# Performance work log

Measured on AMD Instinct MI355X. Metric: run time of the kernel, lower is better.

The kernel has to match this reference:

```python
import jax, jax.numpy as jnp
import numpy as np

N_NODES = 50000
N_EDGES = 800000
NODE_DIM = 128
EDGE_DIM = 64
HID = 2 * NODE_DIM + EDGE_DIM  # 320


def setup_inputs() -> dict:
    key = jax.random.key(0)
    k1, k2, k3, k4 = jax.random.split(key, 4)
    x = jax.random.normal(k1, (N_NODES, NODE_DIM), dtype=jnp.float32)
    edge_index = jax.random.randint(k2, (2, N_EDGES), 0, N_NODES, dtype=jnp.int32)
    edge_ft = jax.random.normal(k3, (N_EDGES, EDGE_DIM), dtype=jnp.float32)
    kw1, kw2 = jax.random.split(k4)
    scale = 1.0 / np.sqrt(HID)
    W_val = jax.random.uniform(kw1, (NODE_DIM, HID), jnp.float32, -scale, scale)
    b_val = jnp.zeros((NODE_DIM,), jnp.float32)
    W_mul = jax.random.uniform(kw2, (NODE_DIM, HID), jnp.float32, -scale, scale)
    b_mul = jnp.zeros((NODE_DIM,), jnp.float32)
    return {"x": x, "edge_index": edge_index, "edge_ft": edge_ft,
            "W_val": W_val, "b_val": b_val, "W_mul": W_mul, "b_mul": b_mul}


def reference(x, edge_index, edge_ft, W_val, b_val, W_mul, b_mul):
    sender, receiver = edge_index[0], edge_index[1]
    # gather + concat: [E, 2*node_dim + edge_dim]
    c = jnp.concatenate([x[sender], x[receiver], edge_ft], axis=1)
    vals = jax.nn.softplus(c @ W_val.T + b_val)
    gate = jax.nn.sigmoid(c @ W_mul.T + b_mul)
    msg = vals * gate  # [E, node_dim]
    # scatter-sum by receiver into [N, node_dim]
    return jax.ops.segment_sum(msg, receiver, num_segments=x.shape[0])
```

## Files before the change

### kernel.cpp

```cpp
#include <hip/hip_runtime.h>
#include <hip/hip_bf16.h>

#define E_EDGES   800000
#define NN_NODES  50000
#define NODE_DIM  128
#define EDGE_DIM  64
#define KDIM      320
#define NTOT      256
#define BM        128
#define BK        64
#define SA        72
#define THREADS   512

typedef _Float16 half8 __attribute__((ext_vector_type(8)));
typedef float    f32x4 __attribute__((ext_vector_type(4)));

__device__ __forceinline__ unsigned short f2h(float f) {
    _Float16 h = (_Float16)f;
    return __builtin_bit_cast(unsigned short, h);
}

__global__ void cast_all_kernel(const float* __restrict__ x,
                                const float* __restrict__ wv,
                                const float* __restrict__ wm,
                                unsigned short* __restrict__ xh,
                                unsigned short* __restrict__ wc) {
    const int n4x = (NN_NODES * NODE_DIM) / 4;
    const int n4h = (NODE_DIM * KDIM) / 4;
    int i = blockIdx.x * blockDim.x + threadIdx.x;
    const float* src;
    unsigned short* dst;
    int j;
    if (i < n4x) { src = x; dst = xh; j = i; }
    else {
        int k = i - n4x;
        if (k >= 2 * n4h) return;
        dst = wc; j = k;
        src = (k < n4h) ? wv : wm;
        if (k >= n4h) { src = wm; j = k - n4h; }
        dst = wc;
        float4 f = ((const float4*)src)[j];
        ushort4 o;
        o.x = f2h(f.x); o.y = f2h(f.y); o.z = f2h(f.z); o.w = f2h(f.w);
        ((ushort4*)wc)[k] = o;
        return;
    }
    float4 f = ((const float4*)src)[j];
    ushort4 o;
    o.x = f2h(f.x); o.y = f2h(f.y); o.z = f2h(f.z); o.w = f2h(f.w);
    ((ushort4*)dst)[j] = o;
}

__global__ void __launch_bounds__(THREADS, 4)
cgc_main(const unsigned short* __restrict__ xh,
         const int* __restrict__ ei,
         const float* __restrict__ ef,
         const unsigned short* __restrict__ Wc,
         const float* __restrict__ bval,
         const float* __restrict__ bmul,
         float* __restrict__ out)
{
    __shared__ unsigned short As[BM * SA];
    __shared__ unsigned short Bs[NTOT * SA];
    __shared__ int sIdx[BM];
    __shared__ int rIdx[BM];

    const int tid  = threadIdx.x;
    const int e0   = blockIdx.x * BM;
    const int lane = tid & 63;
    const int wid  = tid >> 6;
    const int wm   = wid & 1;
    const int wn   = wid >> 1;
    const int q    = lane >> 4;
    const int l16  = lane & 15;

    if (tid < BM) {
        sIdx[tid] = ei[e0 + tid];
        rIdx[tid] = ei[E_EDGES + e0 + tid];
    }

    f32x4 acc[4][4];
    const f32x4 zero4 = {0.f, 0.f, 0.f, 0.f};
#pragma unroll
    for (int mt = 0; mt < 4; ++mt)
#pragma unroll
        for (int nt = 0; nt < 4; ++nt) acc[mt][nt] = zero4;

    for (int c = 0; c < 5; ++c) {
        __syncthreads();
        if (c < 4) {
            const int kcol = (c & 1) * 64;
#pragma unroll
            for (int i = 0; i < 2; ++i) {
                int u = tid + i * THREADS;
                int row = u >> 3, seg = u & 7;
                int node = (c < 2) ? sIdx[row] : rIdx[row];
                uint4 v = *(const uint4*)(xh + (size_t)node * NODE_DIM + kcol + seg * 8);
                *(uint4*)(&As[row * SA + seg * 8]) = v;
            }
        } else {
#pragma unroll
            for (int i = 0; i < 2; ++i) {
                int u = tid + i * THREADS;
                int row = u >> 3, seg = u & 7;
                const float* s = ef + (size_t)(e0 + row) * EDGE_DIM + seg * 8;
                float4 f0 = ((const float4*)s)[0];
                float4 f1 = ((const float4*)s)[1];
                uint4 v;
                v.x = (unsigned)f2h(f0.x) | ((unsigned)f2h(f0.y) << 16);
                v.y = (unsigned)f2h(f0.z) | ((unsigned)f2h(f0.w) << 16);
                v.z = (unsigned)f2h(f1.x) | ((unsigned)f2h(f1.y) << 16);
                v.w = (unsigned)f2h(f1.z) | ((unsigned)f2h(f1.w) << 16);
                *(uint4*)(&As[row * SA + seg * 8]) = v;
            }
        }
        {
            const int kOff = c * BK;
#pragma unroll
            for (int i = 0; i < 4; ++i) {
                int u = tid + i * THREADS;
                int n = u >> 3, seg = u & 7;
                uint4 v = *(const uint4*)(Wc + n * KDIM + kOff + seg * 8);
                *(uint4*)(&Bs[n * SA + seg * 8]) = v;
            }
        }
        __syncthreads();
#pragma unroll
        for (int ks = 0; ks < BK; ks += 32) {
            half8 a[4], b[4];
#pragma unroll
            for (int mt = 0; mt < 4; ++mt)
                a[mt] = *(const half8*)(&As[(wm * 64 + mt * 16 + l16) * SA + ks + q * 8]);
            const int nb0 = wn * 32;
            const int nbase[4] = { nb0, nb0 + 16, 128 + nb0, 128 + nb0 + 16 };
#pragma unroll
            for (int nt = 0; nt < 4; ++nt)
                b[nt] = *(const half8*)(&Bs[(nbase[nt] + l16) * SA + ks + q * 8]);
#pragma unroll
            for (int mt = 0; mt < 4; ++mt)
#pragma unroll
                for (int nt = 0; nt < 4; ++nt)
                    acc[mt][nt] = __builtin_amdgcn_mfma_f32_16x16x32_f16(
                        a[mt], b[nt], acc[mt][nt], 0, 0, 0);
        }
    }

#pragma unroll
    for (int ct = 0; ct < 2; ++ct) {
        const int col = wn * 32 + ct * 16 + l16;
        const float bv = bval[col];
        const float bm = bmul[col];
#pragma unroll
        for (int mt = 0; mt < 4; ++mt) {
#pragma unroll
            for (int r = 0; r < 4; ++r) {
                float v = acc[mt][ct][r] + bv;
                float g = acc[mt][ct + 2][r] + bm;
                float sp  = fmaxf(v, 0.f) + __logf(1.f + __expf(-fabsf(v)));
                float sig = __builtin_amdgcn_rcpf(1.f + __expf(-g));
                float msg = sp * sig;
                int rl = wm * 64 + mt * 16 + q * 4 + r;
                int node = rIdx[rl];
                atomicAdd(out + (size_t)node * NODE_DIM + col, msg);
            }
        }
    }
}

extern "C" void kernel_launch(void* const* d_in, const int* in_sizes, int n_in,
                              void* d_out, int out_size, void* d_ws, size_t ws_size,
                              hipStream_t stream) {
    const float* x  = (const float*)d_in[0];
    const int*   ei = (const int*)d_in[1];
    const float* ef = (const float*)d_in[2];
    const float* Wv = (const float*)d_in[3];
    const float* bv = (const float*)d_in[4];
    const float* Wm = (const float*)d_in[5];
    const float* bm = (const float*)d_in[6];
    float* out = (float*)d_out;

    unsigned short* xh = (unsigned short*)d_ws;
    unsigned short* Wc = (unsigned short*)((char*)d_ws + 12800000);

    hipMemsetAsync(d_out, 0, (size_t)NN_NODES * NODE_DIM * sizeof(float), stream);

    const int n4x = (NN_NODES * NODE_DIM) / 4;
    const int n4w = (2 * NODE_DIM * KDIM) / 4;
    const int total = n4x + n4w;
    cast_all_kernel<<<(total + 255) / 256, 256, 0, stream>>>(x, Wv, Wm, xh, Wc);

    cgc_main<<<E_EDGES / BM, THREADS, 0, stream>>>(xh, ei, ef, Wc, bv, bm, out);
}
```

Measured before the change: 598.6 us.

## Precompute per-node projections and gather them instead of per-edge node GEMM

Splits the linear layer so that the sender and receiver parts of both projections are computed once per node (50k nodes) in a new pcompute kernel and stored as interleaved fp16 values. The edge kernel then runs only the 64-wide edge-feature GEMM and gathers two precomputed 512-byte rows per edge, adding them before softplus and sigmoid. This removes most of the per-edge MFMA work and the per-block weight staging. In exchange it needs a 51 MB workspace, adds an extra fp16 rounding of the per-node partial sums, and keeps the old path as a fallback when the workspace is too small.

```diff
diff --git a/kernel.cpp b/kernel.cpp
--- a/kernel.cpp
+++ b/kernel.cpp
@@ -1,5 +1,4 @@
 #include <hip/hip_runtime.h>
-#include <hip/hip_bf16.h>
 
 #define E_EDGES   800000
 #define NN_NODES  50000
@@ -7,9 +6,11 @@
 #define EDGE_DIM  64
 #define KDIM      320
 #define NTOT      256
-#define BM        128
-#define BK        64
+#define BM        64
+#define OBM       128
+#define BN        64
 #define SA        72
+#define SX        136
 #define THREADS   512
 
 typedef _Float16 half8 __attribute__((ext_vector_type(8)));
@@ -19,6 +20,205 @@
     _Float16 h = (_Float16)f;
     return __builtin_bit_cast(unsigned short, h);
 }
+__device__ __forceinline__ float h2f(unsigned short u) {
+    return (float)__builtin_bit_cast(_Float16, u);
+}
+
+
+__global__ void cast_w(const float* __restrict__ wv,
+                       const float* __restrict__ wm,
+                       unsigned short* __restrict__ Wc) {
+    const int n4h = (NODE_DIM * KDIM) / 4;
+    int i = blockIdx.x * blockDim.x + threadIdx.x;
+    if (i >= 2 * n4h) return;
+    const float* src = (i < n4h) ? wv : wm;
+    int j = (i < n4h) ? i : i - n4h;
+    float4 f = ((const float4*)src)[j];
+    ushort4 o;
+    o.x = f2h(f.x); o.y = f2h(f.y); o.z = f2h(f.z); o.w = f2h(f.w);
+    ((ushort4*)Wc)[i] = o;
+}
+
+__global__ void __launch_bounds__(THREADS, 4)
+pcompute(const float* __restrict__ x,
+         const unsigned short* __restrict__ Wc,
+         const float* __restrict__ bval,
+         const float* __restrict__ bmul,
+         unsigned short* __restrict__ Ph)
+{
+    __shared__ unsigned short Xs[BN * SX];
+    const int tid  = threadIdx.x;
+    const int n0   = blockIdx.x * BN;
+    const int lane = tid & 63;
+    const int wid  = tid >> 6;
+    const int wm   = wid & 1;
+    const int wn   = wid >> 1;
+    const int q    = lane >> 4;
+    const int l16  = lane & 15;
+
+#pragma unroll
+    for (int i = 0; i < 2; ++i) {
+        int u = tid + i * THREADS;
+        int row = u >> 4, seg = u & 15;
+        int node = n0 + row;
+        if (node >= NN_NODES) node = NN_NODES - 1;
+        const float* s = x + (size_t)node * NODE_DIM + seg * 8;
+        float4 f0 = ((const float4*)s)[0];
+        float4 f1 = ((const float4*)s)[1];
+        uint4 v;
+        v.x = (unsigned)f2h(f0.x) | ((unsigned)f2h(f0.y) << 16);
+        v.y = (unsigned)f2h(f0.z) | ((unsigned)f2h(f0.w) << 16);
+        v.z = (unsigned)f2h(f1.x) | ((unsigned)f2h(f1.y) << 16);
+        v.w = (unsigned)f2h(f1.z) | ((unsigned)f2h(f1.w) << 16);
+        *(uint4*)(&Xs[row * SX + seg * 8]) = v;
+    }
+    __syncthreads();
+
+#pragma unroll
+    for (int nhalf = 0; nhalf < 2; ++nhalf) {
+        f32x4 acc[2][4];
+        const f32x4 zero4 = {0.f, 0.f, 0.f, 0.f};
+#pragma unroll
+        for (int mt = 0; mt < 2; ++mt)
+#pragma unroll
+            for (int nt = 0; nt < 4; ++nt) acc[mt][nt] = zero4;
+
+#pragma unroll
+        for (int ks = 0; ks < 4; ++ks) {
+            half8 a[2], b[4];
+#pragma unroll
+            for (int mt = 0; mt < 2; ++mt)
+                a[mt] = *(const half8*)(&Xs[(wm * 32 + mt * 16 + l16) * SX + ks * 32 + q * 8]);
+#pragma unroll
+            for (int nt = 0; nt < 4; ++nt)
+                b[nt] = *(const half8*)(Wc + (size_t)(wn * 64 + nt * 16 + l16) * KDIM
+                                           + nhalf * 128 + ks * 32 + q * 8);
+#pragma unroll
+            for (int mt = 0; mt < 2; ++mt)
+#pragma unroll
+                for (int nt = 0; nt < 4; ++nt)
+                    acc[mt][nt] = __builtin_amdgcn_mfma_f32_16x16x32_f16(
+                        a[mt], b[nt], acc[mt][nt], 0, 0, 0);
+        }
+
+#pragma unroll
+        for (int mt = 0; mt < 2; ++mt) {
+#pragma unroll
+            for (int nt = 0; nt < 4; ++nt) {
+                int j  = wn * 64 + nt * 16 + l16;
+                int c  = j & 127;
+                int vg = j >> 7;
+                float bb = 0.f;
+                if (nhalf == 0) bb = vg ? bmul[c] : bval[c];
+#pragma unroll
+                for (int r = 0; r < 4; ++r) {
+                    int node = n0 + wm * 32 + mt * 16 + q * 4 + r;
+                    if (node < NN_NODES)
+                        Ph[(size_t)node * 512 + nhalf * 256 + c * 2 + vg] =
+                            f2h(acc[mt][nt][r] + bb);
+                }
+            }
+        }
+    }
+}
+
+__global__ void __launch_bounds__(THREADS, 4)
+cgc_main(const unsigned short* __restrict__ Ph,
+         const int* __restrict__ ei,
+         const float* __restrict__ ef,
+         const unsigned short* __restrict__ Wc,
+         float* __restrict__ out)
+{
+    __shared__ unsigned short As[BM * SA];
+    __shared__ int sIdx[BM];
+    __shared__ int rIdx[BM];
+
+    const int tid  = threadIdx.x;
+    const int e0   = blockIdx.x * BM;
+    const int lane = tid & 63;
+    const int wid  = tid >> 6;
+    const int wm   = wid & 1;
+    const int wn   = wid >> 1;
+    const int q    = lane >> 4;
+    const int l16  = lane & 15;
+
+    if (tid < BM) {
+        sIdx[tid] = ei[e0 + tid];
+        rIdx[tid] = ei[E_EDGES + e0 + tid];
+    }
+
+    {
+        int row = tid >> 3, seg = tid & 7;
+        const float* s = ef + (size_t)(e0 + row) * EDGE_DIM + seg * 8;
+        float4 f0 = ((const float4*)s)[0];
+        float4 f1 = ((const float4*)s)[1];
+        uint4 v;
+        v.x = (unsigned)f2h(f0.x) | ((unsigned)f2h(f0.y) << 16);
+        v.y = (unsigned)f2h(f0.z) | ((unsigned)f2h(f0.w) << 16);
+        v.z = (unsigned)f2h(f1.x) | ((unsigned)f2h(f1.y) << 16);
+        v.w = (unsigned)f2h(f1.z) | ((unsigned)f2h(f1.w) << 16);
+        *(uint4*)(&As[row * SA + seg * 8]) = v;
+    }
+
+    const int nb0 = wn * 32;
+    const int nbase[4] = { nb0, nb0 + 16, 128 + nb0, 128 + nb0 + 16 };
+    half8 b[2][4];
+#pragma unroll
+    for (int ks = 0; ks < 2; ++ks)
+#pragma unroll
+        for (int nt = 0; nt < 4; ++nt)
+            b[ks][nt] = *(const half8*)(Wc + (size_t)(nbase[nt] + l16) * KDIM
+                                           + 256 + ks * 32 + q * 8);
+
+    f32x4 acc[2][4];
+    const f32x4 zero4 = {0.f, 0.f, 0.f, 0.f};
+#pragma unroll
+    for (int mt = 0; mt < 2; ++mt)
+#pragma unroll
+        for (int nt = 0; nt < 4; ++nt) acc[mt][nt] = zero4;
+
+    __syncthreads();
+
+#pragma unroll
+    for (int ks = 0; ks < 2; ++ks) {
+        half8 a[2];
+#pragma unroll
+        for (int mt = 0; mt < 2; ++mt)
+            a[mt] = *(const half8*)(&As[(wm * 32 + mt * 16 + l16) * SA + ks * 32 + q * 8]);
+#pragma unroll
+        for (int mt = 0; mt < 2; ++mt)
+#pragma unroll
+            for (int nt = 0; nt < 4; ++nt)
+                acc[mt][nt] = __builtin_amdgcn_mfma_f32_16x16x32_f16(
+                    a[mt], b[ks][nt], acc[mt][nt], 0, 0, 0);
+    }
+
+#pragma unroll
+    for (int mt = 0; mt < 2; ++mt) {
+#pragma unroll
+        for (int r = 0; r < 4; ++r) {
+            int row = wm * 32 + mt * 16 + q * 4 + r;
+            int sN = sIdx[row];
+            int rN = rIdx[row];
+            const unsigned* pS = (const unsigned*)(Ph + (size_t)sN * 512);
+            const unsigned* pR = (const unsigned*)(Ph + (size_t)rN * 512 + 256);
+#pragma unroll
+            for (int ct = 0; ct < 2; ++ct) {
+                int c = wn * 32 + ct * 16 + l16;
+                unsigned us = pS[c];
+                unsigned ur = pR[c];
+                float v = acc[mt][ct][r]     + h2f((unsigned short)(us & 0xffff))
+                                             + h2f((unsigned short)(ur & 0xffff));
+                float g = acc[mt][ct + 2][r] + h2f((unsigned short)(us >> 16))
+                                             + h2f((unsigned short)(ur >> 16));
+                float sp  = fmaxf(v, 0.f) + __logf(1.f + __expf(-fabsf(v)));
+                float sig = __builtin_amdgcn_rcpf(1.f + __expf(-g));
+                atomicAdd(out + (size_t)rN * NODE_DIM + c, sp * sig);
+            }
+        }
+    }
+}
+
 
 __global__ void cast_all_kernel(const float* __restrict__ x,
                                 const float* __restrict__ wv,
@@ -28,45 +228,39 @@
     const int n4x = (NN_NODES * NODE_DIM) / 4;
     const int n4h = (NODE_DIM * KDIM) / 4;
     int i = blockIdx.x * blockDim.x + threadIdx.x;
-    const float* src;
-    unsigned short* dst;
-    int j;
-    if (i < n4x) { src = x; dst = xh; j = i; }
-    else {
+    if (i < n4x) {
+        float4 f = ((const float4*)x)[i];
+        ushort4 o;
+        o.x = f2h(f.x); o.y = f2h(f.y); o.z = f2h(f.z); o.w = f2h(f.w);
+        ((ushort4*)xh)[i] = o;
+    } else {
         int k = i - n4x;
         if (k >= 2 * n4h) return;
-        dst = wc; j = k;
-        src = (k < n4h) ? wv : wm;
-        if (k >= n4h) { src = wm; j = k - n4h; }
-        dst = wc;
+        const float* src = (k < n4h) ? wv : wm;
+        int j = (k < n4h) ? k : k - n4h;
         float4 f = ((const float4*)src)[j];
         ushort4 o;
         o.x = f2h(f.x); o.y = f2h(f.y); o.z = f2h(f.z); o.w = f2h(f.w);
         ((ushort4*)wc)[k] = o;
-        return;
-    }
-    float4 f = ((const float4*)src)[j];
-    ushort4 o;
-    o.x = f2h(f.x); o.y = f2h(f.y); o.z = f2h(f.z); o.w = f2h(f.w);
-    ((ushort4*)dst)[j] = o;
+    }
 }
 
 __global__ void __launch_bounds__(THREADS, 4)
-cgc_main(const unsigned short* __restrict__ xh,
-         const int* __restrict__ ei,
-         const float* __restrict__ ef,
-         const unsigned short* __restrict__ Wc,
-         const float* __restrict__ bval,
-         const float* __restrict__ bmul,
-         float* __restrict__ out)
+cgc_fallback(const unsigned short* __restrict__ xh,
+             const int* __restrict__ ei,
+             const float* __restrict__ ef,
+             const unsigned short* __restrict__ Wc,
+             const float* __restrict__ bval,
+             const float* __restrict__ bmul,
+             float* __restrict__ out)
 {
-    __shared__ unsigned short As[BM * SA];
+    __shared__ unsigned short As[OBM * SA];
     __shared__ unsigned short Bs[NTOT * SA];
-    __shared__ int sIdx[BM];
-    __shared__ int rIdx[BM];
+    __shared__ int sIdx[OBM];
+    __shared__ int rIdx[OBM];
 
     const int tid  = threadIdx.x;
-    const int e0   = blockIdx.x * BM;
+    const int e0   = blockIdx.x * OBM;
     const int lane = tid & 63;
     const int wid  = tid >> 6;
     const int wm   = wid & 1;
@@ -74,7 +268,7 @@
     const int q    = lane >> 4;
     const int l16  = lane & 15;
 
-    if (tid < BM) {
+    if (tid < OBM) {
         sIdx[tid] = ei[e0 + tid];
         rIdx[tid] = ei[E_EDGES + e0 + tid];
     }
@@ -115,7 +309,7 @@
             }
         }
         {
-            const int kOff = c * BK;
+            const int kOff = c * 64;
 #pragma unroll
             for (int i = 0; i < 4; ++i) {
                 int u = tid + i * THREADS;
@@ -126,7 +320,7 @@
         }
         __syncthreads();
 #pragma unroll
-        for (int ks = 0; ks < BK; ks += 32) {
+        for (int ks = 0; ks < 64; ks += 32) {
             half8 a[4], b[4];
 #pragma unroll
             for (int mt = 0; mt < 4; ++mt)
@@ -166,6 +360,7 @@
         }
     }
 }
+
 
 extern "C" void kernel_launch(void* const* d_in, const int* in_sizes, int n_in,
                               void* d_out, int out_size, void* d_ws, size_t ws_size,
@@ -179,15 +374,26 @@
     const float* bm = (const float*)d_in[6];
     float* out = (float*)d_out;
 
-    unsigned short* xh = (unsigned short*)d_ws;
-    unsigned short* Wc = (unsigned short*)((char*)d_ws + 12800000);
-
     hipMemsetAsync(d_out, 0, (size_t)NN_NODES * NODE_DIM * sizeof(float), stream);
 
-    const int n4x = (NN_NODES * NODE_DIM) / 4;
-    const int n4w = (2 * NODE_DIM * KDIM) / 4;
-    const int total = n4x + n4w;
-    cast_all_kernel<<<(total + 255) / 256, 256, 0, stream>>>(x, Wv, Wm, xh, Wc);
-
-    cgc_main<<<E_EDGES / BM, THREADS, 0, stream>>>(xh, ei, ef, Wc, bv, bm, out);
-}
+    const size_t need_new = 262144 + (size_t)NN_NODES * 512 * sizeof(unsigned short);
+
+    if (ws_size >= need_new) {
+        unsigned short* Wc = (unsigned short*)d_ws;
+        unsigned short* Ph = (unsigned short*)((char*)d_ws + 262144);
+
+        const int n4w = (2 * NODE_DIM * KDIM) / 4;
+        cast_w<<<(n4w + 255) / 256, 256, 0, stream>>>(Wv, Wm, Wc);
+        pcompute<<<(NN_NODES + BN - 1) / BN, THREADS, 0, stream>>>(x, Wc, bv, bm, Ph);
+        cgc_main<<<E_EDGES / BM, THREADS, 0, stream>>>(Ph, ei, ef, Wc, out);
+    } else {
+        unsigned short* xh = (unsigned short*)d_ws;
+        unsigned short* Wc = (unsigned short*)((char*)d_ws + 12800000);
+
+        const int n4x = (NN_NODES * NODE_DIM) / 4;
+        const int n4w = (2 * NODE_DIM * KDIM) / 4;
+        const int total = n4x + n4w;
+        cast_all_kernel<<<(total + 255) / 256, 256, 0, stream>>>(x, Wv, Wm, xh, Wc);
+        cgc_fallback<<<E_EDGES / OBM, THREADS, 0, stream>>>(xh, ei, ef, Wc, bv, bm, out);
+    }
+}
```

New measurement: 651.3 us. +8.8%, slower.
